# Kernel tuning notes

Measured on AMD Instinct MI355X. Metric: run time of the kernel, lower is better.

## Reference

```python
import jax, jax.numpy as jnp
import numpy as np

N = 50000   # nodes
E = 800000  # edges
G = 64      # graphs in batch
D = 128     # num_input
H = 128     # num_hidden
O = 10      # num_output


def _linear_params(key, fan_in, fan_out):
    k1, k2 = jax.random.split(key)
    s = 1.0 / np.sqrt(fan_in)
    W = jax.random.uniform(k1, (fan_out, fan_in), jnp.float32, -s, s)
    b = jax.random.uniform(k2, (fan_out,), jnp.float32, -s, s)
    return W, b


def setup_inputs() -> dict:
    key = jax.random.key(0)
    ks = jax.random.split(key, 12)
    x = jax.random.normal(ks[0], (N, D), jnp.float32)
    edge_index = jax.random.randint(ks[1], (2, E), 0, N, dtype=jnp.int32).astype(jnp.int64)
    batch = jnp.sort(jax.random.randint(ks[2], (N,), 0, G, dtype=jnp.int32)).astype(jnp.int64)

    W_rel1, b_rel1 = _linear_params(ks[3], D, H)
    W_root1, _ = _linear_params(ks[4], D, H)
    W_rel2, b_rel2 = _linear_params(ks[5], H, H)
    W_root2, _ = _linear_params(ks[6], H, H)
    W_rel3, b_rel3 = _linear_params(ks[7], H, H)
    W_root3, _ = _linear_params(ks[8], H, H)
    W1, b1 = _linear_params(ks[9], 2 * H, 128)
    W2, b2 = _linear_params(ks[10], 128, 64)
    W3, b3 = _linear_params(ks[11], 64, O)

    return dict(x=x, edge_index=edge_index, batch=batch,
                W_rel1=W_rel1, b_rel1=b_rel1, W_root1=W_root1,
                W_rel2=W_rel2, b_rel2=b_rel2, W_root2=W_root2,
                W_rel3=W_rel3, b_rel3=b_rel3, W_root3=W_root3,
                W1=W1, b1=b1, W2=W2, b2=b2, W3=W3, b3=b3)


def _graph_conv(x, src, dst, W_rel, b_rel, W_root):
    # PyG GraphConv (aggr='add'): out_i = W_rel @ sum_{j->i} x_j + b_rel + W_root @ x_i
    agg = jax.ops.segment_sum(x[src], dst, num_segments=N)  # [N, d]
    return agg @ W_rel.T + b_rel + x @ W_root.T


def _pool(x, batch):
    # concat(global_max_pool, global_mean_pool) -> [G, 2d]
    mx = jax.ops.segment_max(x, batch, num_segments=G)
    mx = jnp.where(jnp.isfinite(mx), mx, 0.0)  # guard empty segments
    sm = jax.ops.segment_sum(x, batch, num_segments=G)
    cnt = jax.ops.segment_sum(jnp.ones((x.shape[0], 1), x.dtype), batch, num_segments=G)
    mean = sm / jnp.maximum(cnt, 1.0)
    return jnp.concatenate([mx, mean], axis=1)


def reference(x, edge_index, batch,
              W_rel1, b_rel1, W_root1,
              W_rel2, b_rel2, W_root2,
              W_rel3, b_rel3, W_root3,
              W1, b1, W2, b2, W3, b3):
    src, dst = edge_index[0], edge_index[1]
    h = jax.nn.relu(_graph_conv(x, src, dst, W_rel1, b_rel1, W_root1))
    x1 = _pool(h, batch)
    h = jax.nn.relu(_graph_conv(h, src, dst, W_rel2, b_rel2, W_root2))
    x2 = _pool(h, batch)
    h = jax.nn.relu(_graph_conv(h, src, dst, W_rel3, b_rel3, W_root3))
    x3 = _pool(h, batch)
    node_embs = h
    graph_emb = x1 + x2 + x3           # [G, 2H]
    z = jax.nn.relu(graph_emb @ W1.T + b1)
    z = jax.nn.relu(z @ W2.T + b2)     # dropout p=0 -> no-op
    logits = z @ W3.T + b3             # [G, O]
    return logits, node_embs, graph_emb
```

## Files before the change

kernel.cpp:

```cpp
#include <hip/hip_runtime.h>
#include <hip/hip_bf16.h>

#define NN 50000
#define EE 800000
#define GG 64
#define NBUCK 196
#define ABLOCKS 125
#define CHUNK 6400
#define BCAP 8192

typedef __attribute__((ext_vector_type(8))) short bf16x8;
typedef __attribute__((ext_vector_type(4))) float f32x4;

__device__ __forceinline__ float bflo(unsigned u) { return __uint_as_float(u << 16); }
__device__ __forceinline__ float bfhi(unsigned u) { return __uint_as_float(u & 0xffff0000u); }
__device__ __forceinline__ float b2f(unsigned short s) { return __uint_as_float(((unsigned)s) << 16); }
__device__ __forceinline__ unsigned short f2bf(float f) {
    __hip_bfloat16 h = __float2bfloat16(f);
    union { __hip_bfloat16 h; unsigned short u; } cv; cv.h = h; return cv.u;
}

__global__ void detect_kernel(const unsigned* __restrict__ xw,
                              const unsigned* __restrict__ eiw,
                              int* __restrict__ flags) {
    __shared__ int s_cnt, s_nz;
    if (threadIdx.x == 0) { s_cnt = 0; s_nz = 0; }
    __syncthreads();
    int cnt = 0;
    for (int i = threadIdx.x; i < 4096; i += 256) {
        unsigned w = xw[(size_t)i * 711];
        unsigned elo = (w >> 7) & 0xFF;
        if (elo >= 100 && elo <= 140) cnt++;
    }
    int nz = 0;
    for (int i = threadIdx.x; i < 1024; i += 256) {
        unsigned w = eiw[(size_t)i * 1560 + 1];
        if (w != 0) nz++;
    }
    atomicAdd(&s_cnt, cnt);
    atomicAdd(&s_nz, nz);
    __syncthreads();
    if (threadIdx.x == 0) {
        flags[0] = (s_cnt < 3600) ? 1 : 0;
        flags[1] = (s_nz  < 8)    ? 1 : 0;
    }
}

struct WPtrs { const void* p[15]; };

__global__ __launch_bounds__(256) void prep_kernel(const void* __restrict__ xsrc,
                                                   const unsigned* __restrict__ eiw,
                                                   WPtrs wp,
                                                   unsigned short* __restrict__ arena,
                                                   int* __restrict__ counts,
                                                   uint4* __restrict__ zero_region,
                                                   const int* __restrict__ flags) {
    const int b = blockIdx.x;
    const int tid = threadIdx.x;
    const int isF32 = flags[0];

    if (b < 3125) {
        const int total4 = NN * 128 / 4;
        for (int i = b * 256 + tid; i < total4; i += 800000) {
            uint2 o;
            if (isF32) {
                float4 f = ((const float4*)xsrc)[i];
                o.x = (unsigned)f2bf(f.x) | ((unsigned)f2bf(f.y) << 16);
                o.y = (unsigned)f2bf(f.z) | ((unsigned)f2bf(f.w) << 16);
            } else {
                o = ((const uint2*)xsrc)[i];
            }
            ((uint2*)arena)[i] = o;
        }
    } else if (b < 3674) {
        const int cnt[15] = {16384,128,16384, 16384,128,16384, 16384,128,16384,
                             32768,128,8192,64,640,10};
        const int dst[15] = {19200000,19232768,19216384, 19232896,19265664,19249280,
                             19265792,19298560,19282176,
                             19298688,19331456,19331584,19339776,19339840,19340480};
        const int total = 140490;
        int i = (b - 3125) * 256 + tid;
        if (i < total) {
            int seg = 0, base = 0;
            while (i - base >= cnt[seg]) { base += cnt[seg]; ++seg; }
            int off = i - base;
            const void* s = wp.p[seg];
            arena[dst[seg] + off] =
                isF32 ? f2bf(((const float*)s)[off]) : ((const unsigned short*)s)[off];
        }
    } else if (b < 3799) {
        __shared__ int hist[256];
        hist[tid] = 0;
        __syncthreads();
        const int i64 = flags[1];
        const int e0 = (b - 3674) * CHUNK;
        for (int it = 0; it < CHUNK / 256; ++it) {
            int e = e0 + it * 256 + tid;
            int d = (int)(i64 ? eiw[(size_t)2 * (EE + e)] : eiw[EE + e]);
            atomicAdd(&hist[d >> 8], 1);
        }
        __syncthreads();
        counts[(b - 3674) * 256 + tid] = hist[tid];
    } else {
        zero_region[(b - 3799) * 256 + tid] = (uint4){0, 0, 0, 0};
    }
}

__global__ __launch_bounds__(256) void bucket_offsets(const int* __restrict__ counts,
                                                      int* __restrict__ offsets,
                                                      int* __restrict__ bucket_base) {
    __shared__ int s[256];
    const int t = threadIdx.x;
    int col = 0;
    for (int b = 0; b < ABLOCKS; ++b) col += counts[b * 256 + t];
    s[t] = col;
    __syncthreads();
    for (int d = 1; d < 256; d <<= 1) {
        int x = (t >= d) ? s[t - d] : 0;
        __syncthreads();
        s[t] += x;
        __syncthreads();
    }
    int base = s[t] - col;
    bucket_base[t] = base;
    if (t == 255) bucket_base[256] = s[255];
    int run = base;
    for (int b = 0; b < ABLOCKS; ++b) {
        offsets[b * 256 + t] = run;
        run += counts[b * 256 + t];
    }
}

__global__ __launch_bounds__(256) void bucket_scatter(const unsigned* __restrict__ eiw,
                                                      const int* __restrict__ offsets,
                                                      unsigned* __restrict__ packed,
                                                      const int* __restrict__ flags) {
    __shared__ int cur[256];
    cur[threadIdx.x] = offsets[blockIdx.x * 256 + threadIdx.x];
    __syncthreads();
    int i64 = flags[1];
    int e0 = blockIdx.x * CHUNK;
    for (int it = 0; it < CHUNK / 256; ++it) {
        int e = e0 + it * 256 + threadIdx.x;
        int s = (int)(i64 ? eiw[(size_t)2 * e]        : eiw[e]);
        int d = (int)(i64 ? eiw[(size_t)2 * (EE + e)] : eiw[EE + e]);
        int pos = atomicAdd(&cur[d >> 8], 1);
        packed[pos] = ((unsigned)s << 8) | (unsigned)(d & 255);
    }
}

__global__ __launch_bounds__(256) void bucket_sort(const unsigned* __restrict__ packed,
                                                   const int* __restrict__ bucket_base,
                                                   int* __restrict__ csr_src,
                                                   int* __restrict__ row_ptr) {
    __shared__ unsigned sbuf[BCAP];
    __shared__ int hist[256];
    __shared__ int cur[256];
    const int t = threadIdx.x;
    const int b = blockIdx.x;
    const int lo = bucket_base[b];
    int n = bucket_base[b + 1] - lo;
    if (n > BCAP) n = BCAP;

    hist[t] = 0;
    __syncthreads();
    for (int i = t; i < n; i += 256) {
        unsigned p = packed[lo + i];
        sbuf[i] = p;
        atomicAdd(&hist[p & 255], 1);
    }
    __syncthreads();
    int v = hist[t];
    __shared__ int s[256];
    s[t] = v;
    __syncthreads();
    for (int d = 1; d < 256; d <<= 1) {
        int x = (t >= d) ? s[t - d] : 0;
        __syncthreads();
        s[t] += x;
        __syncthreads();
    }
    int start = s[t] - v;
    int node = b * 256 + t;
    if (node < NN) row_ptr[node] = lo + start;
    if (b == 0 && t == 0) row_ptr[NN] = EE;
    cur[t] = start;
    __syncthreads();
    for (int i = t; i < n; i += 256) {
        unsigned p = sbuf[i];
        int pos = atomicAdd(&cur[p & 255], 1);
        csr_src[lo + pos] = (int)(p >> 8);
    }
}

__global__ __launch_bounds__(256, 8) void conv_fused(const unsigned short* __restrict__ hin,
                                                     const int* __restrict__ row_ptr,
                                                     const int* __restrict__ csr_src,
                                                     const unsigned short* __restrict__ Wrel,
                                                     const unsigned short* __restrict__ Wroot,
                                                     const unsigned short* __restrict__ brel,
                                                     const unsigned* __restrict__ bw,
                                                     unsigned* __restrict__ pmx,
                                                     float* __restrict__ psum,
                                                     unsigned short* __restrict__ outb,
                                                     void* __restrict__ outG,
                                                     const int* __restrict__ flags) {
    __shared__ __align__(16) unsigned short tile[16][136];
    __shared__ int sbatch[16];

    const int tid  = threadIdx.x;
    const int wv   = tid >> 6;
    const int lane = tid & 63;
    const int half = lane >> 5;
    const int l32  = lane & 31;
    const int m0   = blockIdx.x * 16;
    const uint2* h8 = (const uint2*)hin;

    for (int i = 0; i < 4; ++i) {
        const int lr = wv * 4 + i;
        const int r  = m0 + lr;
        float ax = 0.f, ay = 0.f, az = 0.f, aw = 0.f;
        int jb = row_ptr[r], je = row_ptr[r + 1];
        int j = jb + half;
        for (; j + 14 < je; j += 16) {
            uint2 u[8];
            #pragma unroll
            for (int q = 0; q < 8; ++q)
                u[q] = h8[(size_t)csr_src[j + 2 * q] * 32 + l32];
            #pragma unroll
            for (int q = 0; q < 8; ++q) {
                ax += bflo(u[q].x); ay += bfhi(u[q].x);
                az += bflo(u[q].y); aw += bfhi(u[q].y);
            }
        }
        for (; j + 6 < je; j += 8) {
            uint2 u[4];
            #pragma unroll
            for (int q = 0; q < 4; ++q)
                u[q] = h8[(size_t)csr_src[j + 2 * q] * 32 + l32];
            #pragma unroll
            for (int q = 0; q < 4; ++q) {
                ax += bflo(u[q].x); ay += bfhi(u[q].x);
                az += bflo(u[q].y); aw += bfhi(u[q].y);
            }
        }
        for (; j < je; j += 2) {
            uint2 u = h8[(size_t)csr_src[j] * 32 + l32];
            ax += bflo(u.x); ay += bfhi(u.x);
            az += bflo(u.y); aw += bfhi(u.y);
        }
        ax += __shfl_xor(ax, 32);
        ay += __shfl_xor(ay, 32);
        az += __shfl_xor(az, 32);
        aw += __shfl_xor(aw, 32);
        if (half == 0) {
            uint2 o;
            o.x = (unsigned)f2bf(ax) | ((unsigned)f2bf(ay) << 16);
            o.y = (unsigned)f2bf(az) | ((unsigned)f2bf(aw) << 16);
            *(uint2*)&tile[lr][l32 * 4] = o;
        }
    }
    __syncthreads();

    const int mrow = lane & 15;
    const int quad = lane >> 4;
    const int r    = m0 + mrow;

    f32x4 acc[2];
    acc[0] = (f32x4){0.f, 0.f, 0.f, 0.f};
    acc[1] = (f32x4){0.f, 0.f, 0.f, 0.f};

    #pragma unroll
    for (int kk = 0; kk < 8; ++kk) {
        const unsigned short* Bs = (kk < 4) ? Wrel : Wroot;
        const int kc = (kk & 3) * 32 + quad * 8;
        bf16x8 a;
        if (kk < 4) a = *(const bf16x8*)&tile[mrow][kc];
        else        a = *(const bf16x8*)(hin + (size_t)r * 128 + kc);
        #pragma unroll
        for (int n = 0; n < 2; ++n) {
            const int col0 = (wv * 2 + n) * 16;
            bf16x8 b = *(const bf16x8*)(Bs + (size_t)(col0 + mrow) * 128 + kc);
            acc[n] = __builtin_amdgcn_mfma_f32_16x16x32_bf16(a, b, acc[n], 0, 0, 0);
        }
    }

    __syncthreads();

    const int isF32 = flags[0];
    #pragma unroll
    for (int n = 0; n < 2; ++n) {
        const int col = (wv * 2 + n) * 16 + mrow;
        const float bias = b2f(brel[col]);
        #pragma unroll
        for (int i = 0; i < 4; ++i) {
            const int lrow = quad * 4 + i;
            const int row  = m0 + lrow;
            float v = fmaxf(acc[n][i] + bias, 0.f);
            unsigned short bv = f2bf(v);
            outb[(size_t)row * 128 + col] = bv;
            tile[lrow][col] = bv;
            if (outG) {
                size_t o = (size_t)640 + (size_t)row * 128 + col;
                if (isF32) ((float*)outG)[o] = __uint_as_float((unsigned)bv << 16);
                else       ((unsigned short*)outG)[o] = bv;
            }
        }
    }

    const int i64 = flags[1];
    if (tid < 16) {
        int rr = m0 + tid;
        sbatch[tid] = (int)(i64 ? bw[(size_t)2 * rr] : bw[rr]);
    }
    __syncthreads();
    if (tid < 128) {
        const int col = tid;
        const int slice = blockIdx.x & 7;
        int curg = sbatch[0];
        float mx = 0.f, sm = 0.f;
        for (int rr = 0; rr < 16; ++rr) {
            int g = sbatch[rr];
            if (g != curg) {
                atomicMax(&pmx[(slice * GG + curg) * 128 + col], __float_as_uint(mx));
                unsafeAtomicAdd(&psum[(slice * GG + curg) * 128 + col], sm);
                curg = g; mx = 0.f; sm = 0.f;
            }
            float v = b2f(tile[rr][col]);
            mx = fmaxf(mx, v);
            sm += v;
        }
        atomicMax(&pmx[(slice * GG + curg) * 128 + col], __float_as_uint(mx));
        unsafeAtomicAdd(&psum[(slice * GG + curg) * 128 + col], sm);
    }
}

__global__ __launch_bounds__(256) void mlp_kernel(const unsigned* __restrict__ pmxL,
                                                  const float* __restrict__ psum,
                                                  const unsigned* __restrict__ bw,
                                                  const unsigned short* __restrict__ W1,
                                                  const unsigned short* __restrict__ b1,
                                                  const unsigned short* __restrict__ W2,
                                                  const unsigned short* __restrict__ b2,
                                                  const unsigned short* __restrict__ W3,
                                                  const unsigned short* __restrict__ b3,
                                                  void* __restrict__ out,
                                                  const int* __restrict__ flags) {
    int g = blockIdx.x;
    int t = threadIdx.x;
    int isF32 = flags[0];
    int i64 = flags[1];
    __shared__ float sge[256];
    __shared__ float sz1[128];
    __shared__ float sz2[64];

    int lo = 0, hi = NN;
    while (lo < hi) {
        int mid = (lo + hi) >> 1;
        int bv = (int)(i64 ? bw[(size_t)2 * mid] : bw[mid]);
        if (bv < g) lo = mid + 1; else hi = mid;
    }
    int start = lo;
    hi = NN;
    while (lo < hi) {
        int mid = (lo + hi) >> 1;
        int bv = (int)(i64 ? bw[(size_t)2 * mid] : bw[mid]);
        if (bv < g + 1) lo = mid + 1; else hi = mid;
    }
    int cnt = lo - start;

    float v;
    if (t < 128) {
        v = 0.f;
        #pragma unroll
        for (int L = 0; L < 3; ++L) {
            float m = 0.f;
            #pragma unroll
            for (int s = 0; s < 8; ++s)
                m = fmaxf(m, __uint_as_float(pmxL[((L * 8 + s) * GG + g) * 128 + t]));
            v += m;
        }
    } else {
        float sm = 0.f;
        #pragma unroll
        for (int s = 0; s < 8; ++s) sm += psum[(s * GG + g) * 128 + (t - 128)];
        v = sm / fmaxf((float)cnt, 1.f);
    }
    sge[t] = v;
    size_t geo = (size_t)640 + (size_t)NN * 128 + (size_t)g * 256 + t;
    if (isF32) ((float*)out)[geo] = v;
    else       ((unsigned short*)out)[geo] = f2bf(v);
    __syncthreads();

    if (t < 128) {
        float acc = b2f(b1[t]);
        for (int k = 0; k < 256; ++k) acc = fmaf(sge[k], b2f(W1[t * 256 + k]), acc);
        sz1[t] = fmaxf(acc, 0.f);
    }
    __syncthreads();
    if (t < 64) {
        float acc = b2f(b2[t]);
        for (int k = 0; k < 128; ++k) acc = fmaf(sz1[k], b2f(W2[t * 128 + k]), acc);
        sz2[t] = fmaxf(acc, 0.f);
    }
    __syncthreads();
    if (t < 10) {
        float acc = b2f(b3[t]);
        for (int k = 0; k < 64; ++k) acc = fmaf(sz2[k], b2f(W3[t * 64 + k]), acc);
        size_t o = (size_t)g * 10 + t;
        if (isF32) ((float*)out)[o] = acc;
        else       ((unsigned short*)out)[o] = f2bf(acc);
    }
}

#define XBF_OFF   0
#define HA_OFF    6400000
#define HB_OFF    12800000
#define WR1_OFF   19200000
#define WO1_OFF   19216384
#define BR1_OFF   19232768
#define WR2_OFF   19232896
#define WO2_OFF   19249280
#define BR2_OFF   19265664
#define WR3_OFF   19265792
#define WO3_OFF   19282176
#define BR3_OFF   19298560
#define W1_OFF    19298688
#define B1_OFF    19331456
#define W2_OFF    19331584
#define B2_OFF    19339776
#define W3_OFF    19339840
#define B3_OFF    19340480
#define ARENA_END 19340490

extern "C" void kernel_launch(void* const* d_in, const int* in_sizes, int n_in,
                              void* d_out, int out_size, void* d_ws, size_t ws_size,
                              hipStream_t stream) {
    unsigned short* arena = (unsigned short*)d_ws;
    size_t intBase = ((size_t)ARENA_END * 2 + 255) & ~(size_t)255;
    char* ib = (char*)d_ws + intBase;
    int*      row_ptr = (int*)ib;
    int*      csr_src = (int*)(ib + 200064);
    unsigned* packed  = (unsigned*)(ib + 3400064);
    int*      counts  = (int*)(ib + 6600064);
    int*      offsets = (int*)(ib + 6728064);
    int*      bbase   = (int*)(ib + 6856064);
    unsigned* pmxL    = (unsigned*)(ib + 6857344);
    float*    psum    = (float*)(ib + 7643776);
    int*      flags   = (int*)(ib + 7905920);

    const unsigned* eiw = (const unsigned*)d_in[1];
    const unsigned* bw  = (const unsigned*)d_in[2];
    dim3 blk(256);

    detect_kernel<<<1, 256, 0, stream>>>((const unsigned*)d_in[0], eiw, flags);

    WPtrs wp;
    for (int i = 0; i < 15; ++i) wp.p[i] = d_in[3 + i];
    prep_kernel<<<4055, blk, 0, stream>>>(d_in[0], eiw, wp, arena, counts,
                                          (uint4*)pmxL, flags);

    bucket_offsets<<<1, blk, 0, stream>>>(counts, offsets, bbase);
    bucket_scatter<<<ABLOCKS, blk, 0, stream>>>(eiw, offsets, packed, flags);
    bucket_sort<<<NBUCK, blk, 0, stream>>>(packed, bbase, csr_src, row_ptr);

    const int convGrid = NN / 16;

    conv_fused<<<convGrid, blk, 0, stream>>>(arena + XBF_OFF, row_ptr, csr_src,
                                             arena + WR1_OFF, arena + WO1_OFF, arena + BR1_OFF,
                                             bw, pmxL, psum, arena + HA_OFF, nullptr, flags);
    conv_fused<<<convGrid, blk, 0, stream>>>(arena + HA_OFF, row_ptr, csr_src,
                                             arena + WR2_OFF, arena + WO2_OFF, arena + BR2_OFF,
                                             bw, pmxL + 65536, psum, arena + HB_OFF, nullptr, flags);
    conv_fused<<<convGrid, blk, 0, stream>>>(arena + HB_OFF, row_ptr, csr_src,
                                             arena + WR3_OFF, arena + WO3_OFF, arena + BR3_OFF,
                                             bw, pmxL + 131072, psum, arena + XBF_OFF, d_out, flags);

    mlp_kernel<<<GG, blk, 0, stream>>>(pmxL, psum, bw,
                                       arena + W1_OFF, arena + B1_OFF,
                                       arena + W2_OFF, arena + B2_OFF,
                                       arena + W3_OFF, arena + B3_OFF, d_out, flags);
}
```

Measured before the change: 389.6 us.

## Stage CSR indices in LDS, widen gather to 16B, vectorize output stores

Result: faster. 343.2 us (-11.9%).

```diff
diff --git a/kernel.cpp b/kernel.cpp
--- a/kernel.cpp
+++ b/kernel.cpp
@@ -8,6 +8,7 @@
 #define ABLOCKS 125
 #define CHUNK 6400
 #define BCAP 8192
+#define SPANCAP 512
 
 typedef __attribute__((ext_vector_type(8))) short bf16x8;
 typedef __attribute__((ext_vector_type(4))) float f32x4;
@@ -207,58 +208,90 @@
                                                      const int* __restrict__ flags) {
     __shared__ __align__(16) unsigned short tile[16][136];
     __shared__ int sbatch[16];
+    __shared__ int s_rp[17];
+    __shared__ int s_idx[SPANCAP];
 
     const int tid  = threadIdx.x;
     const int wv   = tid >> 6;
     const int lane = tid & 63;
-    const int half = lane >> 5;
-    const int l32  = lane & 31;
     const int m0   = blockIdx.x * 16;
-    const uint2* h8 = (const uint2*)hin;
-
-    for (int i = 0; i < 4; ++i) {
-        const int lr = wv * 4 + i;
-        const int r  = m0 + lr;
-        float ax = 0.f, ay = 0.f, az = 0.f, aw = 0.f;
-        int jb = row_ptr[r], je = row_ptr[r + 1];
-        int j = jb + half;
-        for (; j + 14 < je; j += 16) {
-            uint2 u[8];
+
+    if (tid < 17) s_rp[tid] = row_ptr[m0 + tid];
+    if (tid >= 32 && tid < 48) {
+        const int i64 = flags[1];
+        int rr = m0 + (tid - 32);
+        sbatch[tid - 32] = (int)(i64 ? bw[(size_t)2 * rr] : bw[rr]);
+    }
+    __syncthreads();
+    const int base = s_rp[0];
+    const int span = s_rp[16] - base;
+    const int nst  = (span < SPANCAP) ? span : SPANCAP;
+    for (int i = tid; i < nst; i += 256) s_idx[i] = csr_src[base + i];
+    __syncthreads();
+
+    const int qd  = lane >> 4;
+    const int l16 = lane & 15;
+    const int lr  = wv * 4 + qd;
+    const int jb  = s_rp[lr]     - base;
+    const int je  = s_rp[lr + 1] - base;
+    const uint4* h16 = (const uint4*)hin;
+
+    float a0 = 0.f, a1 = 0.f, a2 = 0.f, a3 = 0.f,
+          a4 = 0.f, a5 = 0.f, a6 = 0.f, a7 = 0.f;
+
+    if (span <= SPANCAP) {
+        int j = jb;
+        for (; j + 8 <= je; j += 8) {
+            int idx[8];
             #pragma unroll
-            for (int q = 0; q < 8; ++q)
-                u[q] = h8[(size_t)csr_src[j + 2 * q] * 32 + l32];
+            for (int q = 0; q < 8; ++q) idx[q] = s_idx[j + q];
+            uint4 u[8];
+            #pragma unroll
+            for (int q = 0; q < 8; ++q) u[q] = h16[(size_t)idx[q] * 16 + l16];
             #pragma unroll
             for (int q = 0; q < 8; ++q) {
-                ax += bflo(u[q].x); ay += bfhi(u[q].x);
-                az += bflo(u[q].y); aw += bfhi(u[q].y);
+                a0 += bflo(u[q].x); a1 += bfhi(u[q].x);
+                a2 += bflo(u[q].y); a3 += bfhi(u[q].y);
+                a4 += bflo(u[q].z); a5 += bfhi(u[q].z);
+                a6 += bflo(u[q].w); a7 += bfhi(u[q].w);
             }
         }
-        for (; j + 6 < je; j += 8) {
-            uint2 u[4];
+        if (j < je) {
             #pragma unroll
-            for (int q = 0; q < 4; ++q)
-                u[q] = h8[(size_t)csr_src[j + 2 * q] * 32 + l32];
+            for (int q = 0; q < 8; ++q) {
+                int ii = j + q;
+                int ic = (ii < je - 1) ? ii : (je - 1);
+                float sc = (ii < je) ? 1.f : 0.f;
+                uint4 u = h16[(size_t)s_idx[ic] * 16 + l16];
+                a0 = fmaf(bflo(u.x), sc, a0); a1 = fmaf(bfhi(u.x), sc, a1);
+                a2 = fmaf(bflo(u.y), sc, a2); a3 = fmaf(bfhi(u.y), sc, a3);
+                a4 = fmaf(bflo(u.z), sc, a4); a5 = fmaf(bfhi(u.z), sc, a5);
+                a6 = fmaf(bflo(u.w), sc, a6); a7 = fmaf(bfhi(u.w), sc, a7);
+            }
+        }
+    } else {
+        for (int j = jb; j < je; j += 8) {
             #pragma unroll
-            for (int q = 0; q < 4; ++q) {
-                ax += bflo(u[q].x); ay += bfhi(u[q].x);
-                az += bflo(u[q].y); aw += bfhi(u[q].y);
+            for (int q = 0; q < 8; ++q) {
+                int ii = j + q;
+                int ic = (ii < je - 1) ? ii : (je - 1);
+                float sc = (ii < je) ? 1.f : 0.f;
+                uint4 u = h16[(size_t)csr_src[base + ic] * 16 + l16];
+                a0 = fmaf(bflo(u.x), sc, a0); a1 = fmaf(bfhi(u.x), sc, a1);
+                a2 = fmaf(bflo(u.y), sc, a2); a3 = fmaf(bfhi(u.y), sc, a3);
+                a4 = fmaf(bflo(u.z), sc, a4); a5 = fmaf(bfhi(u.z), sc, a5);
+                a6 = fmaf(bflo(u.w), sc, a6); a7 = fmaf(bfhi(u.w), sc, a7);
             }
         }
-        for (; j < je; j += 2) {
-            uint2 u = h8[(size_t)csr_src[j] * 32 + l32];
-            ax += bflo(u.x); ay += bfhi(u.x);
-            az += bflo(u.y); aw += bfhi(u.y);
-        }
-        ax += __shfl_xor(ax, 32);
-        ay += __shfl_xor(ay, 32);
-        az += __shfl_xor(az, 32);
-        aw += __shfl_xor(aw, 32);
-        if (half == 0) {
-            uint2 o;
-            o.x = (unsigned)f2bf(ax) | ((unsigned)f2bf(ay) << 16);
-            o.y = (unsigned)f2bf(az) | ((unsigned)f2bf(aw) << 16);
-            *(uint2*)&tile[lr][l32 * 4] = o;
-        }
+    }
+
+    {
+        uint4 o;
+        o.x = (unsigned)f2bf(a0) | ((unsigned)f2bf(a1) << 16);
+        o.y = (unsigned)f2bf(a2) | ((unsigned)f2bf(a3) << 16);
+        o.z = (unsigned)f2bf(a4) | ((unsigned)f2bf(a5) << 16);
+        o.w = (unsigned)f2bf(a6) | ((unsigned)f2bf(a7) << 16);
+        *(uint4*)&tile[lr][l16 * 8] = o;
     }
     __syncthreads();
 
@@ -287,7 +320,6 @@
 
     __syncthreads();
 
-    const int isF32 = flags[0];
     #pragma unroll
     for (int n = 0; n < 2; ++n) {
         const int col = (wv * 2 + n) * 16 + mrow;
@@ -295,25 +327,30 @@
         #pragma unroll
         for (int i = 0; i < 4; ++i) {
             const int lrow = quad * 4 + i;
-            const int row  = m0 + lrow;
             float v = fmaxf(acc[n][i] + bias, 0.f);
-            unsigned short bv = f2bf(v);
-            outb[(size_t)row * 128 + col] = bv;
-            tile[lrow][col] = bv;
-            if (outG) {
-                size_t o = (size_t)640 + (size_t)row * 128 + col;
-                if (isF32) ((float*)outG)[o] = __uint_as_float((unsigned)bv << 16);
-                else       ((unsigned short*)outG)[o] = bv;
+            tile[lrow][col] = f2bf(v);
+        }
+    }
+    __syncthreads();
+
+    const int isF32 = flags[0];
+    {
+        const int lr2 = tid >> 4;
+        const int c16 = tid & 15;
+        uint4 v = *(const uint4*)&tile[lr2][c16 * 8];
+        ((uint4*)outb)[(size_t)(m0 + lr2) * 16 + c16] = v;
+        if (outG) {
+            if (isF32) {
+                float4* p = (float4*)outG + 160 + (size_t)(m0 + lr2) * 32 + c16 * 2;
+                p[0] = (float4){bflo(v.x), bfhi(v.x), bflo(v.y), bfhi(v.y)};
+                p[1] = (float4){bflo(v.z), bfhi(v.z), bflo(v.w), bfhi(v.w)};
+            } else {
+                uint4* p = (uint4*)((unsigned short*)outG + 640);
+                p[(size_t)(m0 + lr2) * 16 + c16] = v;
             }
         }
     }
 
-    const int i64 = flags[1];
-    if (tid < 16) {
-        int rr = m0 + tid;
-        sbatch[tid] = (int)(i64 ? bw[(size_t)2 * rr] : bw[rr]);
-    }
-    __syncthreads();
     if (tid < 128) {
         const int col = tid;
         const int slice = blockIdx.x & 7;
```
